# Kernel optimization log

Hardware: AMD Instinct MI355X
Metric: run time of the kernel (lower is better)

## Reference

```python
import jax, jax.numpy as jnp
import numpy as np


def setup_inputs() -> dict:
    key = jax.random.key(0)
    k1, k2 = jax.random.split(key)
    x = jax.random.normal(k1, (4, 2048, 2048), dtype=jnp.float32)
    weight = jax.random.normal(k2, (8192, 2048), dtype=jnp.float32) * 0.02
    return {"x": x, "weight": weight, "bits": 8}


def reference(x, weight, bits):
    # ---- activation quantization (per-row int8-style) ----
    scale = jnp.clip(jnp.max(jnp.abs(x), axis=-1, keepdims=True), 1e-5)  # [..., 1]
    max_val = (1 << (bits - 1)) - 1  # 127 for 8 bits
    x_q = jnp.clip(jnp.round(x * (max_val / scale)), -max_val, max_val)

    # ---- ternary weight quantization (-1, 0, 1) ----
    w_scale = jnp.mean(jnp.abs(weight))
    w_q = jnp.where(weight > 0.5 * w_scale, 1.0, 0.0) + jnp.where(
        weight < -0.5 * w_scale, -1.0, 0.0
    )

    # ---- dequantized linear: (x_q @ (w_q * w_scale)^T) / x_scale ----
    out = jnp.einsum("bsi,oi->bso", x_q, w_q * w_scale) / scale

    # ---- squared ReLU ----
    return jnp.maximum(out, 0.0) ** 2
```

## Files before the change

kernel.cpp:

```cpp
#include <hip/hip_runtime.h>
#include <hip/hip_bf16.h>

typedef __attribute__((ext_vector_type(4))) int i32x4;

#define M_DIM 8192
#define N_DIM 8192
#define K_DIM 2048
#define WCOUNT (N_DIM * K_DIM)

__global__ __launch_bounds__(256) void k_abs_partial(const float* __restrict__ w,
                                                     float* __restrict__ part) {
    int tid = blockIdx.x * 256 + threadIdx.x;
    const float4* w4 = (const float4*)w;
    float s = 0.0f;
    const int total4 = WCOUNT / 4;
    for (int i = tid; i < total4; i += 2048 * 256) {
        float4 v = w4[i];
        s += fabsf(v.x) + fabsf(v.y) + fabsf(v.z) + fabsf(v.w);
    }
    #pragma unroll
    for (int off = 1; off < 64; off <<= 1) s += __shfl_xor(s, off);
    __shared__ float red[4];
    if ((threadIdx.x & 63) == 0) red[threadIdx.x >> 6] = s;
    __syncthreads();
    if (threadIdx.x == 0)
        part[blockIdx.x] = (red[0] + red[1]) + (red[2] + red[3]);
}

__global__ __launch_bounds__(256) void k_abs_final(const float* __restrict__ part,
                                                   float* __restrict__ sum) {
    int t = threadIdx.x;
    float s = 0.0f;
    #pragma unroll
    for (int i = 0; i < 8; i++) s += part[t + i * 256];
    #pragma unroll
    for (int off = 1; off < 64; off <<= 1) s += __shfl_xor(s, off);
    __shared__ float red[4];
    if ((t & 63) == 0) red[t >> 6] = s;
    __syncthreads();
    if (t == 0) sum[0] = (red[0] + red[1]) + (red[2] + red[3]);
}

__global__ __launch_bounds__(256) void k_wquant(const float* __restrict__ w,
                                                const float* __restrict__ sum,
                                                unsigned int* __restrict__ wq) {
    const float thr = 0.5f * (sum[0] * (1.0f / 16777216.0f));
    int tid = blockIdx.x * 256 + threadIdx.x;
    const float4* w4 = (const float4*)w;
    const int total4 = WCOUNT / 4;
    for (int i = tid; i < total4; i += 2048 * 256) {
        float4 v = w4[i];
        union { signed char c[4]; unsigned int u; } q;
        q.c[0] = v.x > thr ? 1 : (v.x < -thr ? -1 : 0);
        q.c[1] = v.y > thr ? 1 : (v.y < -thr ? -1 : 0);
        q.c[2] = v.z > thr ? 1 : (v.z < -thr ? -1 : 0);
        q.c[3] = v.w > thr ? 1 : (v.w < -thr ? -1 : 0);
        wq[i] = q.u;
    }
}

__global__ __launch_bounds__(256) void k_xquant(const float* __restrict__ x,
                                                signed char* __restrict__ xq,
                                                float* __restrict__ scale) {
    const int row = blockIdx.x;
    const int t = threadIdx.x;
    const float4* xr = (const float4*)(x + (size_t)row * K_DIM);
    float4 a = xr[t * 2];
    float4 b = xr[t * 2 + 1];
    float m = fmaxf(fmaxf(fmaxf(fabsf(a.x), fabsf(a.y)), fmaxf(fabsf(a.z), fabsf(a.w))),
                    fmaxf(fmaxf(fabsf(b.x), fabsf(b.y)), fmaxf(fabsf(b.z), fabsf(b.w))));
    #pragma unroll
    for (int off = 1; off < 64; off <<= 1) m = fmaxf(m, __shfl_xor(m, off));
    __shared__ float red[4];
    if ((t & 63) == 0) red[t >> 6] = m;
    __syncthreads();
    m = fmaxf(fmaxf(red[0], red[1]), fmaxf(red[2], red[3]));
    const float sc = fmaxf(m, 1e-5f);
    if (t == 0) scale[row] = sc;
    const float r = 127.0f / sc;
    float q[8] = {a.x, a.y, a.z, a.w, b.x, b.y, b.z, b.w};
    union { signed char c[8]; uint2 v; } pk;
    #pragma unroll
    for (int j = 0; j < 8; j++) {
        float v = rintf(q[j] * r);
        v = fminf(fmaxf(v, -127.0f), 127.0f);
        pk.c[j] = (signed char)v;
    }
    *(uint2*)(xq + (size_t)row * K_DIM + t * 8) = pk.v;
}

#define GLDS16(g, l)                                                                   \
    __builtin_amdgcn_global_load_lds((const __attribute__((address_space(1))) void*)(g), \
                                     (__attribute__((address_space(3))) void*)(l), 16, 0, 0)

__global__ __launch_bounds__(256) void k_gemm(const signed char* __restrict__ Aq,
                                              const signed char* __restrict__ Bq,
                                              const float* __restrict__ scale,
                                              const float* __restrict__ sum,
                                              float* __restrict__ out) {
    __shared__ signed char As[128 * 64];
    __shared__ signed char Bs[128 * 64];

    const int t = threadIdx.x;
    const int lane = t & 63;
    const int wid = t >> 6;
    const int wr = wid >> 1;
    const int wc = wid & 1;
    const int brow = blockIdx.y;
    const int bcol = blockIdx.x;

    const int c0 = t, c1 = t + 256;
    const int g0 = ((c0 & 3) ^ ((c0 >> 3) & 3)) * 16;
    const int g1 = ((c1 & 3) ^ ((c1 >> 3) & 3)) * 16;
    const signed char* ga0 = Aq + (size_t)(brow * 128 + (c0 >> 2)) * K_DIM + g0;
    const signed char* ga1 = Aq + (size_t)(brow * 128 + (c1 >> 2)) * K_DIM + g1;
    const signed char* gb0 = Bq + (size_t)(bcol * 128 + (c0 >> 2)) * K_DIM + g0;
    const signed char* gb1 = Bq + (size_t)(bcol * 128 + (c1 >> 2)) * K_DIM + g1;
    signed char* lA0 = As + wid * 1024;
    signed char* lA1 = As + 4096 + wid * 1024;
    signed char* lB0 = Bs + wid * 1024;
    signed char* lB1 = Bs + 4096 + wid * 1024;

    i32x4 zero = {0, 0, 0, 0};
    i32x4 acc[4][4];
    #pragma unroll
    for (int m = 0; m < 4; m++)
        #pragma unroll
        for (int n = 0; n < 4; n++) acc[m][n] = zero;

    const int swz = ((lane >> 4) ^ ((lane >> 1) & 3)) * 16;
    const int a_off = (wr * 64 + (lane & 15)) * 64 + swz;
    const int b_off = (wc * 64 + (lane & 15)) * 64 + swz;

    for (int kt = 0; kt < K_DIM; kt += 64) {
        GLDS16(ga0, lA0);
        GLDS16(ga1, lA1);
        GLDS16(gb0, lB0);
        GLDS16(gb1, lB1);
        ga0 += 64; ga1 += 64; gb0 += 64; gb1 += 64;
        __syncthreads();

        i32x4 af[4], bfr[4];
        #pragma unroll
        for (int m = 0; m < 4; m++) af[m] = *(const i32x4*)&As[a_off + m * 1024];
        #pragma unroll
        for (int n = 0; n < 4; n++) bfr[n] = *(const i32x4*)&Bs[b_off + n * 1024];
        #pragma unroll
        for (int m = 0; m < 4; m++)
            #pragma unroll
            for (int n = 0; n < 4; n++)
                acc[m][n] = __builtin_amdgcn_mfma_i32_16x16x64_i8(af[m], bfr[n], acc[m][n], 0, 0, 0);
        __syncthreads();
    }

    const float wsc = sum[0] * (1.0f / 16777216.0f);
    const int rbase = brow * 128 + wr * 64 + ((lane >> 4) * 4);
    const int cbase = bcol * 128 + wc * 64 + (lane & 15);
    #pragma unroll
    for (int m = 0; m < 4; m++) {
        #pragma unroll
        for (int j = 0; j < 4; j++) {
            const int grow = rbase + m * 16 + j;
            const float coef = wsc / scale[grow];
            #pragma unroll
            for (int n = 0; n < 4; n++) {
                float v = (float)acc[m][n][j] * coef;
                v = fmaxf(v, 0.0f);
                out[(size_t)grow * N_DIM + cbase + n * 16] = v * v;
            }
        }
    }
}

extern "C" void kernel_launch(void* const* d_in, const int* in_sizes, int n_in,
                              void* d_out, int out_size, void* d_ws, size_t ws_size,
                              hipStream_t stream) {
    const float* x = (const float*)d_in[0];
    const float* w = (const float*)d_in[1];
    float* out = (float*)d_out;

    char* ws = (char*)d_ws;
    float* sum   = (float*)ws;
    float* part  = (float*)(ws + 256);
    float* scale = (float*)(ws + 16384);
    signed char* xq = (signed char*)(ws + 65536);
    signed char* wq = (signed char*)(ws + 65536 + 16777216);

    k_abs_partial<<<2048, 256, 0, stream>>>(w, part);
    k_abs_final<<<1, 256, 0, stream>>>(part, sum);
    k_wquant<<<2048, 256, 0, stream>>>(w, sum, (unsigned int*)wq);
    k_xquant<<<M_DIM, 256, 0, stream>>>(x, xq, scale);
    k_gemm<<<dim3(N_DIM / 128, M_DIM / 128), 256, 0, stream>>>(xq, wq, scale, sum, out);
}
```

Before: 223.7 us.

## Restructure int8 GEMM with 128x256 tiles, 32x32 MFMA, double-buffered LDS

Rewrites the int8 GEMM to use 512-thread blocks with 128x256 output tiles, 32x32x32 int8 MFMAs and a double-buffered LDS pipeline with explicit vmcnt waits and barriers. The block-to-tile mapping is remapped so blocks on the same XCD share A rows. Per-row coefficients move to a small precompute kernel, and output stores become nontemporal. The goal is to hide global-load latency and raise MFMA utilisation. The cost is more LDS per block, higher register pressure and hand-tuned wait counts that could be fragile.

Result: faster. 195.3 us (-12.7%).

```diff
diff --git a/kernel.cpp b/kernel.cpp
--- a/kernel.cpp
+++ b/kernel.cpp
@@ -2,6 +2,7 @@
 #include <hip/hip_bf16.h>
 
 typedef __attribute__((ext_vector_type(4))) int i32x4;
+typedef __attribute__((ext_vector_type(16))) int i32x16;
 
 #define M_DIM 8192
 #define N_DIM 8192
@@ -89,87 +90,126 @@
     *(uint2*)(xq + (size_t)row * K_DIM + t * 8) = pk.v;
 }
 
+__global__ __launch_bounds__(256) void k_coef(const float* __restrict__ sum,
+                                              const float* __restrict__ scale,
+                                              float* __restrict__ coef) {
+    const int i = blockIdx.x * 256 + threadIdx.x;
+    coef[i] = (sum[0] * (1.0f / 16777216.0f)) / scale[i];
+}
+
 #define GLDS16(g, l)                                                                   \
     __builtin_amdgcn_global_load_lds((const __attribute__((address_space(1))) void*)(g), \
                                      (__attribute__((address_space(3))) void*)(l), 16, 0, 0)
 
-__global__ __launch_bounds__(256) void k_gemm(const signed char* __restrict__ Aq,
-                                              const signed char* __restrict__ Bq,
-                                              const float* __restrict__ scale,
-                                              const float* __restrict__ sum,
-                                              float* __restrict__ out) {
-    __shared__ signed char As[128 * 64];
-    __shared__ signed char Bs[128 * 64];
+#define BAR __builtin_amdgcn_s_barrier()
+#define VMCNT3 asm volatile("s_waitcnt vmcnt(3)" ::: "memory")
+#define VMCNT0 asm volatile("s_waitcnt vmcnt(0)" ::: "memory")
+#define ABUF(b) ((b) * 24576)
+#define BBUF(b) ((b) * 24576 + 8192)
+
+__global__ __launch_bounds__(512, 4) void k_gemm(const signed char* __restrict__ Aq,
+                                                 const signed char* __restrict__ Bq,
+                                                 const float* __restrict__ coef,
+                                                 float* __restrict__ out) {
+    __shared__ signed char lds[49152];
 
     const int t = threadIdx.x;
     const int lane = t & 63;
     const int wid = t >> 6;
-    const int wr = wid >> 1;
-    const int wc = wid & 1;
-    const int brow = blockIdx.y;
-    const int bcol = blockIdx.x;
-
-    const int c0 = t, c1 = t + 256;
-    const int g0 = ((c0 & 3) ^ ((c0 >> 3) & 3)) * 16;
-    const int g1 = ((c1 & 3) ^ ((c1 >> 3) & 3)) * 16;
-    const signed char* ga0 = Aq + (size_t)(brow * 128 + (c0 >> 2)) * K_DIM + g0;
-    const signed char* ga1 = Aq + (size_t)(brow * 128 + (c1 >> 2)) * K_DIM + g1;
-    const signed char* gb0 = Bq + (size_t)(bcol * 128 + (c0 >> 2)) * K_DIM + g0;
-    const signed char* gb1 = Bq + (size_t)(bcol * 128 + (c1 >> 2)) * K_DIM + g1;
-    signed char* lA0 = As + wid * 1024;
-    signed char* lA1 = As + 4096 + wid * 1024;
-    signed char* lB0 = Bs + wid * 1024;
-    signed char* lB1 = Bs + 4096 + wid * 1024;
-
-    i32x4 zero = {0, 0, 0, 0};
-    i32x4 acc[4][4];
-    #pragma unroll
-    for (int m = 0; m < 4; m++)
+    const int wm = wid >> 2;
+    const int wn = wid & 3;
+    const int l31 = lane & 31;
+    const int kg = lane >> 5;
+
+    const int bid = blockIdx.x;
+    const int xcd = bid & 7;
+    const int idx = bid >> 3;
+    const int bcol = (idx >> 5) * 4 + (idx & 3);
+    const int brow = xcd * 8 + ((idx >> 2) & 7);
+
+    const int g4 = ((t & 3) ^ ((t >> 3) & 3)) << 4;
+    const int arow_s = t >> 2;
+    const int dstc = wid * 1024;
+
+    const signed char* Abase = Aq + (size_t)(brow * 128) * K_DIM;
+    const signed char* Bbase = Bq + (size_t)(bcol * 256) * K_DIM;
+
+#define STG_K(buf, kt) do {                                                        \
+        GLDS16(Abase + arow_s * K_DIM + (kt) * 64 + g4, lds + ABUF(buf) + dstc);   \
+        GLDS16(Bbase + arow_s * K_DIM + (kt) * 64 + g4, lds + BBUF(buf) + dstc);   \
+        GLDS16(Bbase + (128 + arow_s) * K_DIM + (kt) * 64 + g4,                    \
+               lds + BBUF(buf) + 8192 + dstc); } while (0)
+
+    const int rs = (l31 >> 1) & 3;
+    const int ko0 = ((0 + kg) ^ rs) << 4;
+    const int ko1 = ((2 + kg) ^ rs) << 4;
+    const int aoff = (wm * 64 + l31) * 64;
+    const int boff = 8192 + (wn * 64 + l31) * 64;
+
+    i32x16 acc00 = (i32x16){0,0,0,0,0,0,0,0,0,0,0,0,0,0,0,0};
+    i32x16 acc01 = acc00, acc10 = acc00, acc11 = acc00;
+
+#define KTILE(buf) do {                                                            \
+        const int ab = (buf) * 24576 + aoff;                                       \
+        const int bb = (buf) * 24576 + boff;                                       \
+        i32x4 a00 = *(const i32x4*)&lds[ab + ko0];                                 \
+        i32x4 a10 = *(const i32x4*)&lds[ab + 2048 + ko0];                          \
+        i32x4 b00 = *(const i32x4*)&lds[bb + ko0];                                 \
+        i32x4 b10 = *(const i32x4*)&lds[bb + 2048 + ko0];                          \
+        i32x4 a01 = *(const i32x4*)&lds[ab + ko1];                                 \
+        i32x4 a11 = *(const i32x4*)&lds[ab + 2048 + ko1];                          \
+        i32x4 b01 = *(const i32x4*)&lds[bb + ko1];                                 \
+        i32x4 b11 = *(const i32x4*)&lds[bb + 2048 + ko1];                          \
+        __builtin_amdgcn_s_setprio(1);                                             \
+        acc00 = __builtin_amdgcn_mfma_i32_32x32x32_i8(a00, b00, acc00, 0, 0, 0);   \
+        acc01 = __builtin_amdgcn_mfma_i32_32x32x32_i8(a00, b10, acc01, 0, 0, 0);   \
+        acc10 = __builtin_amdgcn_mfma_i32_32x32x32_i8(a10, b00, acc10, 0, 0, 0);   \
+        acc11 = __builtin_amdgcn_mfma_i32_32x32x32_i8(a10, b10, acc11, 0, 0, 0);   \
+        acc00 = __builtin_amdgcn_mfma_i32_32x32x32_i8(a01, b01, acc00, 0, 0, 0);   \
+        acc01 = __builtin_amdgcn_mfma_i32_32x32x32_i8(a01, b11, acc01, 0, 0, 0);   \
+        acc10 = __builtin_amdgcn_mfma_i32_32x32x32_i8(a11, b01, acc10, 0, 0, 0);   \
+        acc11 = __builtin_amdgcn_mfma_i32_32x32x32_i8(a11, b11, acc11, 0, 0, 0);   \
+        __builtin_amdgcn_s_setprio(0); } while (0)
+
+    STG_K(0, 0);
+    STG_K(1, 1);
+    VMCNT3;
+    BAR;
+
+    #pragma unroll 1
+    for (int i = 0; i < 16; i++) {
+        const int kt = 2 * i;
+        KTILE(0);
+        BAR;
+        if (i < 15) { STG_K(0, kt + 2); VMCNT3; }
+        else        { VMCNT0; }
+        BAR;
+        KTILE(1);
+        if (i < 15) {
+            BAR;
+            STG_K(1, kt + 3); VMCNT3;
+            BAR;
+        }
+    }
+
+    const int rb = brow * 128 + wm * 64 + 4 * kg;
+    const int cb = bcol * 256 + wn * 64 + l31;
+    #pragma unroll
+    for (int mt = 0; mt < 2; mt++) {
+        const i32x16 ac0 = mt ? acc10 : acc00;
+        const i32x16 ac1 = mt ? acc11 : acc01;
         #pragma unroll
-        for (int n = 0; n < 4; n++) acc[m][n] = zero;
-
-    const int swz = ((lane >> 4) ^ ((lane >> 1) & 3)) * 16;
-    const int a_off = (wr * 64 + (lane & 15)) * 64 + swz;
-    const int b_off = (wc * 64 + (lane & 15)) * 64 + swz;
-
-    for (int kt = 0; kt < K_DIM; kt += 64) {
-        GLDS16(ga0, lA0);
-        GLDS16(ga1, lA1);
-        GLDS16(gb0, lB0);
-        GLDS16(gb1, lB1);
-        ga0 += 64; ga1 += 64; gb0 += 64; gb1 += 64;
-        __syncthreads();
-
-        i32x4 af[4], bfr[4];
-        #pragma unroll
-        for (int m = 0; m < 4; m++) af[m] = *(const i32x4*)&As[a_off + m * 1024];
-        #pragma unroll
-        for (int n = 0; n < 4; n++) bfr[n] = *(const i32x4*)&Bs[b_off + n * 1024];
-        #pragma unroll
-        for (int m = 0; m < 4; m++)
-            #pragma unroll
-            for (int n = 0; n < 4; n++)
-                acc[m][n] = __builtin_amdgcn_mfma_i32_16x16x64_i8(af[m], bfr[n], acc[m][n], 0, 0, 0);
-        __syncthreads();
-    }
-
-    const float wsc = sum[0] * (1.0f / 16777216.0f);
-    const int rbase = brow * 128 + wr * 64 + ((lane >> 4) * 4);
-    const int cbase = bcol * 128 + wc * 64 + (lane & 15);
-    #pragma unroll
-    for (int m = 0; m < 4; m++) {
-        #pragma unroll
-        for (int j = 0; j < 4; j++) {
-            const int grow = rbase + m * 16 + j;
-            const float coef = wsc / scale[grow];
-            #pragma unroll
-            for (int n = 0; n < 4; n++) {
-                float v = (float)acc[m][n][j] * coef;
-                v = fmaxf(v, 0.0f);
-                out[(size_t)grow * N_DIM + cbase + n * 16] = v * v;
-            }
+        for (int r = 0; r < 16; r++) {
+            const int grow = rb + mt * 32 + (r & 3) + 8 * (r >> 2);
+            const float c = coef[grow];
+            float v0 = (float)ac0[r] * c; v0 = fmaxf(v0, 0.0f);
+            float v1 = (float)ac1[r] * c; v1 = fmaxf(v1, 0.0f);
+            __builtin_nontemporal_store(v0 * v0, &out[(size_t)grow * N_DIM + cb]);
+            __builtin_nontemporal_store(v1 * v1, &out[(size_t)grow * N_DIM + cb + 32]);
         }
     }
+#undef STG_K
+#undef KTILE
 }
 
 extern "C" void kernel_launch(void* const* d_in, const int* in_sizes, int n_in,
@@ -183,12 +223,14 @@
     float* sum   = (float*)ws;
     float* part  = (float*)(ws + 256);
     float* scale = (float*)(ws + 16384);
-    signed char* xq = (signed char*)(ws + 65536);
-    signed char* wq = (signed char*)(ws + 65536 + 16777216);
+    float* coef  = (float*)(ws + 49152);
+    signed char* xq = (signed char*)(ws + 131072);
+    signed char* wq = (signed char*)(ws + 131072 + 16777216);
 
     k_abs_partial<<<2048, 256, 0, stream>>>(w, part);
     k_abs_final<<<1, 256, 0, stream>>>(part, sum);
     k_wquant<<<2048, 256, 0, stream>>>(w, sum, (unsigned int*)wq);
     k_xquant<<<M_DIM, 256, 0, stream>>>(x, xq, scale);
-    k_gemm<<<dim3(N_DIM / 128, M_DIM / 128), 256, 0, stream>>>(xq, wq, scale, sum, out);
-}
+    k_coef<<<32, 256, 0, stream>>>(sum, scale, coef);
+    k_gemm<<<dim3(2048), 512, 0, stream>>>(xq, wq, coef, out);
+}
```
